# Performance work log

Hardware: AMD Instinct MI355X
Metric: run time of the kernel (lower is better)

## Reference

```python
import jax, jax.numpy as jnp
import numpy as np

N, DIM = 100000, 512
HID = DIM // 2


def _mlp(z, W1, b1, W2, b2):
    # shared scorer: [N, dim] -> [N, 1]
    h = jax.nn.relu(z @ W1 + b1)
    return h @ W2 + b2


def setup_inputs() -> dict:
    key = jax.random.key(0)
    k1, k2, k3, k4 = jax.random.split(key, 4)
    s1 = 1.0 / np.sqrt(DIM)
    s2 = 1.0 / np.sqrt(HID)
    return {
        "z1": jax.random.normal(k1, (N, DIM), dtype=jnp.float32),
        "z2": jax.random.normal(k2, (N, DIM), dtype=jnp.float32),
        "W1": jax.random.normal(k3, (DIM, HID), dtype=jnp.float32) * s1,
        "b1": jnp.zeros((HID,), dtype=jnp.float32),
        "W2": jax.random.normal(k4, (HID, 1), dtype=jnp.float32) * s2,
        "b2": jnp.zeros((1,), dtype=jnp.float32),
    }


def reference(z1, z2, W1, b1, W2, b2):
    x = _mlp(z1, W1, b1, W2, b2)  # [N, 1]
    y = _mlp(z2, W1, b1, W2, b2)  # [N, 1]
    # exp-normalize pair: score_x = e^x / (e^x + e^y) == sigmoid(x - y)
    # computed exactly as in the original (plain exp, no max-subtract)
    e_x = jnp.exp(x)
    e_y = jnp.exp(y)
    denom = e_x + e_y
    score_x = e_x / denom  # [N, 1]
    score_y = e_y / denom  # [N, 1]
    # diag(score) @ z  ==  score * z  (row-wise broadcast scale)
    return score_x * z1 + score_y * z2
```

## Files before the change

### kernel.cpp

```cpp
#include <hip/hip_runtime.h>
#include <hip/hip_bf16.h>
#include <cmath>

#define DIM 512
#define HID 256
#define ROWS_PB 32
#define NCHUNK 16
#define CB 16384

typedef __attribute__((ext_vector_type(8))) short short8;
typedef __attribute__((ext_vector_type(4))) float f32x4;
typedef __attribute__((ext_vector_type(16))) float f32x16;
typedef __attribute__((ext_vector_type(4))) unsigned int u32x4;

__device__ __forceinline__ unsigned short f2bf(float f) {
  union { float f; unsigned u; } v; v.f = f;
  unsigned u = v.u;
  return (unsigned short)((u + 0x7FFFu + ((u >> 16) & 1u)) >> 16);
}
__device__ __forceinline__ float bf2f(short h) {
  union { unsigned u; float f; } v;
  v.u = ((unsigned)(unsigned short)h) << 16;
  return v.f;
}

__global__ void w1_swz_kernel(const float* __restrict__ W1,
                              unsigned short* __restrict__ w1s) {
  int tid = blockIdx.x * blockDim.x + threadIdx.x;
  if (tid >= DIM * HID) return;
  int k = tid / HID;
  int c = tid - k * HID;
  w1s[(((k >> 3) * HID) + c) * 8 + (k & 7)] = f2bf(W1[tid]);
}

__device__ __forceinline__ short8 cvt8(const f32x4 p0, const f32x4 p1) {
  short8 r;
  r[0] = (short)f2bf(p0[0]); r[1] = (short)f2bf(p0[1]);
  r[2] = (short)f2bf(p0[2]); r[3] = (short)f2bf(p0[3]);
  r[4] = (short)f2bf(p1[0]); r[5] = (short)f2bf(p1[1]);
  r[6] = (short)f2bf(p1[2]); r[7] = (short)f2bf(p1[3]);
  return r;
}

__device__ __forceinline__ void wcombine(float wa, const short8 a, float wb,
                                         const short8 b, f32x4& o0, f32x4& o1) {
#pragma unroll
  for (int i = 0; i < 4; ++i) {
    o0[i] = wa * bf2f(a[i]) + wb * bf2f(b[i]);
    o1[i] = wa * bf2f(a[i + 4]) + wb * bf2f(b[i + 4]);
  }
}

__global__ __launch_bounds__(256, 2) void fa_main_kernel(
    const float* __restrict__ z1, const float* __restrict__ z2,
    const unsigned short* __restrict__ w1s,
    const float* __restrict__ bias1, const float* __restrict__ W2,
    const float* __restrict__ bias2, float* __restrict__ out, int n) {
  __shared__ char smem[81920];
  short8* Az = (short8*)smem;
  char* Bs = smem + 65536;
  float* xs2 = (float*)(smem + 65536);

  const int t = threadIdx.x;
  const int w = t >> 6;
  const int l = t & 63;
  const int l15 = l & 15, l16 = l >> 4;
  const int l31 = l & 31, lhi = l >> 5;
  const int s = w & 1;
  const int h = w >> 1;
  const int row0 = blockIdx.x * ROWS_PB;
  const int myrow = row0 + h * 16 + l15;
  const bool rok = myrow < n;
  const float* zz = s ? z2 : z1;
  const float* ap = zz + (size_t)myrow * DIM + (l16 << 3);
  const f32x4 zf4 = (f32x4){0.f, 0.f, 0.f, 0.f};

  u32x4 breg0, breg1, breg2, breg3;
#define BLOAD(c)                                            \
  {                                                         \
    const u32x4* g = (const u32x4*)w1s + (c) * 1024 + t;    \
    breg0 = g[0];                                           \
    breg1 = g[256];                                         \
    breg2 = g[512];                                         \
    breg3 = g[768];                                         \
  }
#define BWRITE()                                            \
  {                                                         \
    u32x4* d = (u32x4*)Bs + t;                              \
    d[0] = breg0;                                           \
    d[256] = breg1;                                         \
    d[512] = breg2;                                         \
    d[768] = breg3;                                         \
  }

  BLOAD(0);
  __builtin_amdgcn_sched_barrier(0);
#pragma unroll
  for (int g = 0; g < 4; ++g) {
    f32x4 p[4][2];
#pragma unroll
    for (int j = 0; j < 4; ++j) {
      const float* pp = ap + (((g << 2) + j) << 5);
      p[j][0] = rok ? *(const f32x4*)(pp) : zf4;
      p[j][1] = rok ? *(const f32x4*)(pp + 4) : zf4;
    }
#pragma unroll
    for (int j = 0; j < 4; ++j)
      Az[((s * NCHUNK + (g << 2) + j) * 2 + h) * 64 + l] =
          cvt8(p[j][0], p[j][1]);
  }
  BWRITE();
  __syncthreads();

  f32x16 acc[4];
#pragma unroll
  for (int g = 0; g < 4; ++g)
#pragma unroll
    for (int r = 0; r < 16; ++r) acc[g][r] = 0.f;

  const int aTl = (l31 >> 4);
  const int aLo = (l & 15);
  const int bBase = (h << 2) * 32 + l31;

#pragma unroll
  for (int c = 0; c < NCHUNK; ++c) {
    if (c + 1 < NCHUNK) BLOAD(c + 1);
    __builtin_amdgcn_sched_barrier(0);
    const short8* azc = Az + ((s * NCHUNK + c) * 2 + aTl) * 64 + aLo;
    const short8* bsc = (const short8*)Bs;
#pragma unroll
    for (int ks = 0; ks < 2; ++ks) {
      const short8 af = azc[((ks << 1) + lhi) << 4];
      const short8* bp = bsc + (((ks << 1) + lhi) << 8) + bBase;
#pragma unroll
      for (int g = 0; g < 4; ++g) {
        const short8 bf = bp[g << 5];
        acc[g] = __builtin_amdgcn_mfma_f32_32x32x16_bf16(af, bf, acc[g], 0, 0,
                                                         0);
      }
    }
    __syncthreads();
    if (c + 1 < NCHUNK) BWRITE();
    __syncthreads();
  }

  float part[16];
#pragma unroll
  for (int r = 0; r < 16; ++r) part[r] = 0.f;
#pragma unroll
  for (int g = 0; g < 4; ++g) {
    const int cc = ((h << 2) + g) * 32 + l31;
    const float w2v = W2[cc];
    const float b1v = bias1[cc];
#pragma unroll
    for (int r = 0; r < 16; ++r) {
      const float hh = acc[g][r] + b1v;
      part[r] += (hh > 0.f) ? hh * w2v : 0.f;
    }
  }
#pragma unroll
  for (int r = 0; r < 16; ++r) {
#pragma unroll
    for (int m = 1; m < 32; m <<= 1) part[r] += __shfl_xor(part[r], m, 64);
  }
  if (l31 == 0) {
#pragma unroll
    for (int r = 0; r < 16; ++r) {
      const int row = (r & 3) + ((r >> 2) << 3) + (lhi << 2);
      xs2[(s * 2 + h) * 32 + row] = part[r];
    }
  }
  __syncthreads();

  const int tl2 = w & 1;
  const int orow_l = tl2 * 16 + l15;
  const int grow = row0 + orow_l;
  const float x = xs2[0 * 32 + orow_l] + xs2[1 * 32 + orow_l];
  const float y = xs2[2 * 32 + orow_l] + xs2[3 * 32 + orow_l];
  const float sx = 1.f / (1.f + __expf(y - x));
  const float sy = 1.f - sx;
  float* orow = out + (size_t)grow * DIM + (l16 << 3);
  if (grow < n) {
#pragma unroll
    for (int j = 0; j < 8; ++j) {
      const int cc = ((w >> 1) << 3) + j;
      const short8 a0 = Az[((0 * NCHUNK + cc) * 2 + tl2) * 64 + l];
      const short8 a1 = Az[((1 * NCHUNK + cc) * 2 + tl2) * 64 + l];
      f32x4 o0, o1;
      wcombine(sx, a0, sy, a1, o0, o1);
      *(f32x4*)(orow + (cc << 5)) = o0;
      *(f32x4*)(orow + (cc << 5) + 4) = o1;
    }
  }
#undef BLOAD
#undef BWRITE
}

extern "C" void kernel_launch(void* const* d_in, const int* in_sizes, int n_in,
                              void* d_out, int out_size, void* d_ws,
                              size_t ws_size, hipStream_t stream) {
  const float* z1 = (const float*)d_in[0];
  const float* z2 = (const float*)d_in[1];
  const float* W1 = (const float*)d_in[2];
  const float* b1 = (const float*)d_in[3];
  const float* W2 = (const float*)d_in[4];
  const float* b2 = (const float*)d_in[5];
  float* out = (float*)d_out;
  const int n = in_sizes[0] / DIM;
  unsigned short* w1s = (unsigned short*)d_ws;

  hipLaunchKernelGGL(w1_swz_kernel, dim3((DIM * HID + 255) / 256), dim3(256),
                     0, stream, W1, w1s);
  const int nwg = (n + ROWS_PB - 1) / ROWS_PB;
  hipLaunchKernelGGL(fa_main_kernel, dim3(nwg), dim3(256), 0, stream, z1, z2,
                     w1s, b1, W2, b2, out, n);
}
```

Before: 200.4 us.

## Stream A fragments from registers, double-buffer W1 via direct global-to-LDS loads

Drops the 64KB LDS staging of the bf16-converted z rows. Each wave now prefetches its A fragments two chunks ahead into registers and converts them just before the MFMAs. W1 chunks are double-buffered in LDS with global_load_lds, which removes the register round-trip and one barrier per chunk. The smaller LDS footprint allows raising launch bounds to 3 blocks per CU. In exchange, the epilogue rereads z1 and z2 from global memory in fp32 instead of reusing the bf16 copy, which adds memory traffic but likely hits cache and gives full-precision output.

```diff
diff --git a/kernel.cpp b/kernel.cpp
--- a/kernel.cpp
+++ b/kernel.cpp
@@ -11,17 +11,11 @@
 typedef __attribute__((ext_vector_type(8))) short short8;
 typedef __attribute__((ext_vector_type(4))) float f32x4;
 typedef __attribute__((ext_vector_type(16))) float f32x16;
-typedef __attribute__((ext_vector_type(4))) unsigned int u32x4;
 
 __device__ __forceinline__ unsigned short f2bf(float f) {
   union { float f; unsigned u; } v; v.f = f;
   unsigned u = v.u;
   return (unsigned short)((u + 0x7FFFu + ((u >> 16) & 1u)) >> 16);
-}
-__device__ __forceinline__ float bf2f(short h) {
-  union { unsigned u; float f; } v;
-  v.u = ((unsigned)(unsigned short)h) << 16;
-  return v.f;
 }
 
 __global__ void w1_swz_kernel(const float* __restrict__ W1,
@@ -42,95 +36,94 @@
   return r;
 }
 
-__device__ __forceinline__ void wcombine(float wa, const short8 a, float wb,
-                                         const short8 b, f32x4& o0, f32x4& o1) {
-#pragma unroll
-  for (int i = 0; i < 4; ++i) {
-    o0[i] = wa * bf2f(a[i]) + wb * bf2f(b[i]);
-    o1[i] = wa * bf2f(a[i + 4]) + wb * bf2f(b[i + 4]);
-  }
-}
-
-__global__ __launch_bounds__(256, 2) void fa_main_kernel(
+__global__ __launch_bounds__(256, 3) void fa_main_kernel(
     const float* __restrict__ z1, const float* __restrict__ z2,
     const unsigned short* __restrict__ w1s,
     const float* __restrict__ bias1, const float* __restrict__ W2,
     const float* __restrict__ bias2, float* __restrict__ out, int n) {
-  __shared__ char smem[81920];
-  short8* Az = (short8*)smem;
-  char* Bs = smem + 65536;
-  float* xs2 = (float*)(smem + 65536);
+  __shared__ char Bs[2][CB];
+  __shared__ float xs2[4][32];
 
   const int t = threadIdx.x;
   const int w = t >> 6;
   const int l = t & 63;
-  const int l15 = l & 15, l16 = l >> 4;
   const int l31 = l & 31, lhi = l >> 5;
   const int s = w & 1;
   const int h = w >> 1;
   const int row0 = blockIdx.x * ROWS_PB;
-  const int myrow = row0 + h * 16 + l15;
+  const int myrow = row0 + l31;
   const bool rok = myrow < n;
   const float* zz = s ? z2 : z1;
-  const float* ap = zz + (size_t)myrow * DIM + (l16 << 3);
+  const float* ap = zz + (size_t)myrow * DIM + (lhi << 3);
   const f32x4 zf4 = (f32x4){0.f, 0.f, 0.f, 0.f};
 
-  u32x4 breg0, breg1, breg2, breg3;
-#define BLOAD(c)                                            \
-  {                                                         \
-    const u32x4* g = (const u32x4*)w1s + (c) * 1024 + t;    \
-    breg0 = g[0];                                           \
-    breg1 = g[256];                                         \
-    breg2 = g[512];                                         \
-    breg3 = g[768];                                         \
-  }
-#define BWRITE()                                            \
-  {                                                         \
-    u32x4* d = (u32x4*)Bs + t;                              \
-    d[0] = breg0;                                           \
-    d[256] = breg1;                                         \
-    d[512] = breg2;                                         \
-    d[768] = breg3;                                         \
-  }
-
-  BLOAD(0);
-  __builtin_amdgcn_sched_barrier(0);
-#pragma unroll
-  for (int g = 0; g < 4; ++g) {
-    f32x4 p[4][2];
-#pragma unroll
-    for (int j = 0; j < 4; ++j) {
-      const float* pp = ap + (((g << 2) + j) << 5);
-      p[j][0] = rok ? *(const f32x4*)(pp) : zf4;
-      p[j][1] = rok ? *(const f32x4*)(pp + 4) : zf4;
-    }
-#pragma unroll
-    for (int j = 0; j < 4; ++j)
-      Az[((s * NCHUNK + (g << 2) + j) * 2 + h) * 64 + l] =
-          cvt8(p[j][0], p[j][1]);
-  }
-  BWRITE();
+  auto STAGE = [&](int cc, int buf) {
+    const char* gsrc = (const char*)w1s + cc * CB + l * 16;
+    char* ldst = (char*)&Bs[buf][0];
+#pragma unroll
+    for (int r = 0; r < 4; ++r) {
+      const int rr = w + r * 4;
+      __builtin_amdgcn_global_load_lds(
+          (const __attribute__((address_space(1))) void*)(gsrc + rr * 1024),
+          (__attribute__((address_space(3))) void*)(ldst + rr * 1024), 16, 0,
+          0);
+    }
+  };
+
+  STAGE(0, 0);
+  f32x4 pa0[2][2], pa1[2][2];
+#pragma unroll
+  for (int ks = 0; ks < 2; ++ks) {
+    const float* p0 = ap + (ks << 4);
+    pa0[ks][0] = rok ? *(const f32x4*)(p0) : zf4;
+    pa0[ks][1] = rok ? *(const f32x4*)(p0 + 4) : zf4;
+    const float* p1 = ap + 32 + (ks << 4);
+    pa1[ks][0] = rok ? *(const f32x4*)(p1) : zf4;
+    pa1[ks][1] = rok ? *(const f32x4*)(p1 + 4) : zf4;
+  }
+
+  f32x16 acc[4];
+#pragma unroll
+  for (int g = 0; g < 4; ++g)
+#pragma unroll
+    for (int r = 0; r < 16; ++r) acc[g][r] = 0.f;
+
+  const int bBase = ((h << 2) << 5) + l31;
+
   __syncthreads();
 
-  f32x16 acc[4];
-#pragma unroll
-  for (int g = 0; g < 4; ++g)
-#pragma unroll
-    for (int r = 0; r < 16; ++r) acc[g][r] = 0.f;
-
-  const int aTl = (l31 >> 4);
-  const int aLo = (l & 15);
-  const int bBase = (h << 2) * 32 + l31;
-
 #pragma unroll
   for (int c = 0; c < NCHUNK; ++c) {
-    if (c + 1 < NCHUNK) BLOAD(c + 1);
+    short8 af0, af1;
+    if (c & 1) {
+      af0 = cvt8(pa1[0][0], pa1[0][1]);
+      af1 = cvt8(pa1[1][0], pa1[1][1]);
+    } else {
+      af0 = cvt8(pa0[0][0], pa0[0][1]);
+      af1 = cvt8(pa0[1][0], pa0[1][1]);
+    }
+    if (c + 1 < NCHUNK) STAGE(c + 1, (c + 1) & 1);
+    if (c + 2 < NCHUNK) {
+      const float* apn = ap + ((c + 2) << 5);
+      if (c & 1) {
+#pragma unroll
+        for (int ks = 0; ks < 2; ++ks) {
+          pa1[ks][0] = rok ? *(const f32x4*)(apn + (ks << 4)) : zf4;
+          pa1[ks][1] = rok ? *(const f32x4*)(apn + (ks << 4) + 4) : zf4;
+        }
+      } else {
+#pragma unroll
+        for (int ks = 0; ks < 2; ++ks) {
+          pa0[ks][0] = rok ? *(const f32x4*)(apn + (ks << 4)) : zf4;
+          pa0[ks][1] = rok ? *(const f32x4*)(apn + (ks << 4) + 4) : zf4;
+        }
+      }
+    }
     __builtin_amdgcn_sched_barrier(0);
-    const short8* azc = Az + ((s * NCHUNK + c) * 2 + aTl) * 64 + aLo;
-    const short8* bsc = (const short8*)Bs;
+    const short8* bsc = (const short8*)&Bs[c & 1][0];
 #pragma unroll
     for (int ks = 0; ks < 2; ++ks) {
-      const short8 af = azc[((ks << 1) + lhi) << 4];
+      const short8 af = ks ? af1 : af0;
       const short8* bp = bsc + (((ks << 1) + lhi) << 8) + bBase;
 #pragma unroll
       for (int g = 0; g < 4; ++g) {
@@ -140,8 +133,6 @@
       }
     }
     __syncthreads();
-    if (c + 1 < NCHUNK) BWRITE();
-    __syncthreads();
   }
 
   float part[16];
@@ -167,33 +158,35 @@
 #pragma unroll
     for (int r = 0; r < 16; ++r) {
       const int row = (r & 3) + ((r >> 2) << 3) + (lhi << 2);
-      xs2[(s * 2 + h) * 32 + row] = part[r];
+      xs2[(s << 1) + h][row] = part[r];
     }
   }
   __syncthreads();
 
-  const int tl2 = w & 1;
-  const int orow_l = tl2 * 16 + l15;
-  const int grow = row0 + orow_l;
-  const float x = xs2[0 * 32 + orow_l] + xs2[1 * 32 + orow_l];
-  const float y = xs2[2 * 32 + orow_l] + xs2[3 * 32 + orow_l];
-  const float sx = 1.f / (1.f + __expf(y - x));
-  const float sy = 1.f - sx;
-  float* orow = out + (size_t)grow * DIM + (l16 << 3);
-  if (grow < n) {
-#pragma unroll
-    for (int j = 0; j < 8; ++j) {
-      const int cc = ((w >> 1) << 3) + j;
-      const short8 a0 = Az[((0 * NCHUNK + cc) * 2 + tl2) * 64 + l];
-      const short8 a1 = Az[((1 * NCHUNK + cc) * 2 + tl2) * 64 + l];
-      f32x4 o0, o1;
-      wcombine(sx, a0, sy, a1, o0, o1);
-      *(f32x4*)(orow + (cc << 5)) = o0;
-      *(f32x4*)(orow + (cc << 5) + 4) = o1;
-    }
-  }
-#undef BLOAD
-#undef BWRITE
+#pragma unroll
+  for (int j = 0; j < 8; ++j) {
+    const int rl = (w << 3) + j;
+    const int grow = row0 + rl;
+    if (grow < n) {
+      const float x = xs2[0][rl] + xs2[1][rl];
+      const float y = xs2[2][rl] + xs2[3][rl];
+      const float sx = 1.f / (1.f + __expf(y - x));
+      const float sy = 1.f - sx;
+      const size_t off = (size_t)grow * DIM + (l << 2);
+#pragma unroll
+      for (int half = 0; half < 2; ++half) {
+        const size_t o = off + (half << 8);
+        const f32x4 a4 = *(const f32x4*)(z1 + o);
+        const f32x4 b4 = *(const f32x4*)(z2 + o);
+        f32x4 ov;
+        ov[0] = sx * a4[0] + sy * b4[0];
+        ov[1] = sx * a4[1] + sy * b4[1];
+        ov[2] = sx * a4[2] + sy * b4[2];
+        ov[3] = sx * a4[3] + sy * b4[3];
+        *(f32x4*)(out + o) = ov;
+      }
+    }
+  }
 }
 
 extern "C" void kernel_launch(void* const* d_in, const int* in_sizes, int n_in,
```

Result: slower. 238.6 us (+19.0%).
